# Performance work log

Hardware: AMD Instinct MI355X
Metric: run time of the kernel (lower is better)

The kernel has to match this reference:

```python
import jax, jax.numpy as jnp
import numpy as np

E = 1024
H = 16
D = E // H  # head dim 64
B = 2
S = 2048


def setup_inputs() -> dict:
    key = jax.random.key(0)
    k1, k2, k3, k4, k5 = jax.random.split(key, 5)
    scale = 1.0 / np.sqrt(E)
    return {
        "x": jax.random.normal(k1, (B, S, E), dtype=jnp.float32),
        "W_in": jax.random.normal(k2, (E, 3 * E), dtype=jnp.float32) * scale,
        "b_in": jnp.zeros((3 * E,), dtype=jnp.float32),
        "W_out": jax.random.normal(k3, (E, E), dtype=jnp.float32) * scale,
        "b_out": jnp.zeros((E,), dtype=jnp.float32),
        "causal_mask": 1,
    }


def reference(x, W_in, b_in, W_out, b_out, causal_mask):
    b, s, e = x.shape
    qkv = x @ W_in + b_in                      # [B,S,3E]
    q, k, v = jnp.split(qkv, 3, axis=-1)
    # [B,S,E] -> [B,H,S,D]
    q = q.reshape(b, s, H, D).transpose(0, 2, 1, 3)
    k = k.reshape(b, s, H, D).transpose(0, 2, 1, 3)
    v = v.reshape(b, s, H, D).transpose(0, 2, 1, 3)
    scores = jnp.einsum("bhqd,bhkd->bhqk", q, k)
    if causal_mask:
        # mask applied before scaling in the original; -inf is scale-invariant
        mask = jnp.triu(jnp.ones((s, s), dtype=bool), k=1)
        scores = jnp.where(mask, -jnp.inf, scores)
    scores = scores / np.sqrt(D)
    weight = jax.nn.softmax(scores, axis=-1)
    out = jnp.einsum("bhqk,bhkd->bhqd", weight, v)   # [B,H,S,D]
    out = out.transpose(0, 2, 1, 3).reshape(b, s, e)
    return out @ W_out + b_out
```

## Files before the change

### kernel.cpp

```cpp
#include <hip/hip_runtime.h>
#include <hip/hip_bf16.h>
#include <cmath>

typedef __bf16 bf16;
typedef __attribute__((ext_vector_type(8))) __bf16 bf16x8;
typedef __attribute__((ext_vector_type(4))) __bf16 bf16x4;
typedef __attribute__((ext_vector_type(4))) float f32x4;
typedef __attribute__((ext_vector_type(16))) float f32x16;
typedef unsigned int u32;

constexpr int S  = 2048;
constexpr int E  = 1024;
constexpr int H  = 16;
constexpr int D  = 64;
constexpr int B  = 2;
constexpr int M  = B * S;
constexpr int N3 = 3 * E;
constexpr int NROWS = B * H * S;

static __device__ __forceinline__ void gload16(const void* g, void* l) {
  __builtin_amdgcn_global_load_lds((const __attribute__((address_space(1))) void*)g,
                                   (__attribute__((address_space(3))) void*)l, 16, 0, 0);
}

static __device__ __forceinline__ u32 pack2(float a, float b) {
  union { bf16 h[2]; u32 u; } r;
  r.h[0] = (bf16)a; r.h[1] = (bf16)b;
  return r.u;
}
typedef union { u32 w[4]; bf16x8 v; } FU;

__global__ void k_cvt(const float* __restrict__ in, bf16* __restrict__ out) {
  const int i = (blockIdx.x * blockDim.x + threadIdx.x) * 4;
  const float4 v = *(const float4*)(in + i);
  bf16x4 o = { (bf16)v.x, (bf16)v.y, (bf16)v.z, (bf16)v.w };
  *(bf16x4*)(out + i) = o;
}

__global__ void k_transpose_cvt(const float* __restrict__ in, bf16* __restrict__ out,
                                int R, int C) {
  __shared__ float t[32][33];
  const int c0 = blockIdx.x * 32, r0 = blockIdx.y * 32;
  const int tx = threadIdx.x, ty = threadIdx.y;
  #pragma unroll
  for (int j = 0; j < 32; j += 8)
    t[ty + j][tx] = in[(size_t)(r0 + ty + j) * C + c0 + tx];
  __syncthreads();
  #pragma unroll
  for (int j = 0; j < 32; j += 8)
    out[(size_t)(c0 + ty + j) * R + r0 + tx] = (bf16)t[tx][ty + j];
}

template<int EPI>
__global__ __launch_bounds__(256) void k_gemm(
    const bf16* __restrict__ A, const bf16* __restrict__ Bt,
    const float* __restrict__ bias, float* __restrict__ outF,
    bf16* __restrict__ oQ, bf16* __restrict__ oK, bf16* __restrict__ oV,
    int Kdim, int Nn)
{
  __shared__ __align__(16) char smem[65536];
  const int tid = threadIdx.x;
  const int lane = tid & 63, w = tid >> 6;
  const int lane15 = lane & 15, quad = lane >> 4;
  const int wm = w >> 1, wn = w & 1;

  const int nbx = Nn >> 7;
  const int nwg = gridDim.x;
  const int bid = blockIdx.x;
  const int swz = (bid & 7) * (nwg >> 3) + (bid >> 3);
  const int bn0 = (swz % nbx) * 128;
  const int bm0 = (swz / nbx) * 128;

  const int so0 = w * 1024 + lane * 16;
  int srow[4], slk[4];
  #pragma unroll
  for (int p = 0; p < 4; ++p) {
    const int o = p * 4096 + so0;
    const int row = o >> 7, cbyte = o & 127;
    srow[p] = row;
    slk[p] = (cbyte ^ ((row & 7) << 4)) >> 1;
  }

  f32x4 acc[4][4] = {};
  const int nkt = Kdim >> 6;

  #pragma unroll
  for (int p = 0; p < 4; ++p) {
    gload16(A  + (size_t)(bm0 + srow[p]) * Kdim + slk[p], smem +         p * 4096 + w * 1024);
    gload16(Bt + (size_t)(bn0 + srow[p]) * Kdim + slk[p], smem + 32768 + p * 4096 + w * 1024);
  }

  #pragma unroll 1
  for (int kt = 0; kt < nkt; ++kt) {
    const int cur = kt & 1;
    __builtin_amdgcn_s_barrier();
    if (kt + 1 < nkt) {
      const int k0 = (kt + 1) << 6;
      const int nb = (cur ^ 1) * 16384;
      #pragma unroll
      for (int p = 0; p < 4; ++p) {
        gload16(A  + (size_t)(bm0 + srow[p]) * Kdim + k0 + slk[p],
                smem + nb +         p * 4096 + w * 1024);
        gload16(Bt + (size_t)(bn0 + srow[p]) * Kdim + k0 + slk[p],
                smem + nb + 32768 + p * 4096 + w * 1024);
      }
      asm volatile("s_waitcnt vmcnt(8)" ::: "memory");
    } else {
      asm volatile("s_waitcnt vmcnt(0)" ::: "memory");
    }
    __builtin_amdgcn_s_barrier();

    const char* cA = smem + cur * 16384;
    const char* cB = smem + 32768 + cur * 16384;
    #pragma unroll
    for (int kk = 0; kk < 2; ++kk) {
      bf16x8 af[4], bfr[4];
      #pragma unroll
      for (int f = 0; f < 4; ++f) {
        const int ra = wm * 64 + f * 16 + lane15;
        af[f] = *(const bf16x8*)(cA + ra * 128 +
                 ((kk * 64 + (quad << 4)) ^ ((ra & 7) << 4)));
        const int rb = wn * 64 + f * 16 + lane15;
        bfr[f] = *(const bf16x8*)(cB + rb * 128 +
                 ((kk * 64 + (quad << 4)) ^ ((rb & 7) << 4)));
      }
      #pragma unroll
      for (int i = 0; i < 4; ++i)
        #pragma unroll
        for (int j = 0; j < 4; ++j)
          acc[i][j] = __builtin_amdgcn_mfma_f32_16x16x32_bf16(af[i], bfr[j], acc[i][j], 0, 0, 0);
    }
  }

  if constexpr (EPI == 1) {
    #pragma unroll
    for (int i = 0; i < 4; ++i)
      #pragma unroll
      for (int j = 0; j < 4; ++j) {
        const int n = bn0 + wn * 64 + j * 16 + lane15;
        const float bv = bias[n];
        #pragma unroll
        for (int r = 0; r < 4; ++r) {
          const int m = bm0 + wm * 64 + i * 16 + quad * 4 + r;
          outF[(size_t)m * E + n] = acc[i][j][r] + bv;
        }
      }
  } else {
    const int which = bn0 >> 10;
    const int b  = bm0 >> 11;
    const int s0 = bm0 & (S - 1);
    const int cn0 = bn0 & (E - 1);
    if (which < 2) {
      __builtin_amdgcn_s_barrier();
      char* lC = smem;
      #pragma unroll
      for (int j = 0; j < 4; ++j) {
        const int n_loc = wn * 64 + j * 16 + lane15;
        const float bv = bias[bn0 + n_loc];
        #pragma unroll
        for (int i = 0; i < 4; ++i)
          #pragma unroll
          for (int r = 0; r < 4; ++r) {
            const int m_loc = wm * 64 + i * 16 + quad * 4 + r;
            *(bf16*)(lC + m_loc * 256 + ((n_loc * 2) ^ ((m_loc & 7) << 4))) =
                (bf16)(acc[i][j][r] + bv);
          }
      }
      __builtin_amdgcn_s_barrier();
      const int h0 = cn0 >> 6;
      #pragma unroll
      for (int it = 0; it < 8; ++it) {
        const int cch = w * 64 + it * 8 + (lane >> 3);
        const int m_loc = cch >> 1, hh = cch & 1, piece = lane & 7;
        const bf16x8 vv = *(const bf16x8*)(lC + m_loc * 256 +
                          ((hh * 128 + piece * 16) ^ ((m_loc & 7) << 4)));
        if (which == 0) {
          *(bf16x8*)(oQ + ((size_t)(b * H + h0 + hh) * S + s0 + m_loc) * D + piece * 8) = vv;
        } else {
          const size_t hb = (size_t)(b * H + h0 + hh) * S * D;
          const int tile = (s0 + m_loc) >> 6;
          const int row = m_loc & 63;
          *(bf16x8*)(oK + hb + (size_t)tile * 4096 + (piece >> 1) * 1024 +
                     (row >> 5) * 512 + (32 * (piece & 1) + (row & 31)) * 8) = vv;
        }
      }
    } else {
      #pragma unroll
      for (int j = 0; j < 4; ++j) {
        const int n_loc = wn * 64 + j * 16 + lane15;
        const int cn = cn0 + n_loc;
        const int hv = cn >> 6, dd = cn & 63;
        const float bv = bias[bn0 + n_loc];
        const size_t hb = (size_t)(b * H + hv) * S * D;
        #pragma unroll
        for (int i = 0; i < 4; ++i) {
          const int scol_g = s0 + wm * 64 + i * 16 + quad * 4;
          const int vtile = scol_g >> 6;
          const int cg = (scol_g & 63) >> 3;
          bf16x4 pk = { (bf16)(acc[i][j][0] + bv), (bf16)(acc[i][j][1] + bv),
                        (bf16)(acc[i][j][2] + bv), (bf16)(acc[i][j][3] + bv) };
          *(bf16x4*)(oV + hb + (size_t)vtile * 4096 + (cg >> 1) * 1024 +
                     (dd >> 5) * 512 + (32 * (cg & 1) + (dd & 31)) * 8 +
                     (quad & 1) * 4) = pk;
        }
      }
    }
  }
}

__global__ __launch_bounds__(256, 2) void k_attn(
    const bf16* __restrict__ Qb, const bf16* __restrict__ Kf, const bf16* __restrict__ Vf,
    bf16* __restrict__ pO0, bf16* __restrict__ pO1,
    float* __restrict__ pM, float* __restrict__ pL, const int* __restrict__ cmask)
{
  __shared__ float corr_lds[4][32];
  __shared__ float lrow_lds[4][32];

  const int tid = threadIdx.x, lane = tid & 63, w = tid >> 6;
  const int h = lane >> 5, q31 = lane & 31;
  const int bh = blockIdx.x;
  const int jb = blockIdx.y;
  const int causal = cmask[0];
  const float S2 = 0.18033688011112042f;

  const bf16* Qh = Qb + (size_t)bh * S * D;
  const bf16* Kh = Kf + (size_t)bh * S * D;
  const bf16* Vh = Vf + (size_t)bh * S * D;

  #pragma unroll 1
  for (int pidx = 0; pidx < 2; ++pidx) {
    const int c  = pidx ? (15 - jb) : jb;
    const int t0 = causal ? (pidx ? (c + 1) : 0) : (pidx ? 16 : 0);
    const int t1 = causal ? (pidx ? (2 * c + 2) : (c + 1)) : (pidx ? 32 : 16);
    const int q0w = c * 128 + 32 * w;
    const int qg  = q0w + q31;
    const int t1w = causal ? min(t1, (q0w + 31) / 64 + 1) : t1;

    bf16x8 qf[4];
    #pragma unroll
    for (int ds = 0; ds < 4; ++ds)
      qf[ds] = *(const bf16x8*)(Qh + (size_t)qg * D + 16 * ds + 8 * h);

    f32x16 o0 = {}, o1 = {};
    float mrun = -INFINITY, lr = 0.f;

    #pragma unroll 1
    for (int t = t0; t < t1w; ++t) {
      const bf16* ktb = Kh + (size_t)t * 4096;
      const bf16* vtb = Vh + (size_t)t * 4096;

      bf16x8 kf0[4], kf1[4];
      #pragma unroll
      for (int ds = 0; ds < 4; ++ds) {
        kf0[ds] = *(const bf16x8*)(ktb + ds * 1024 +       lane * 8);
        kf1[ds] = *(const bf16x8*)(ktb + ds * 1024 + 512 + lane * 8);
      }

      f32x16 s0v = {}, s1v = {};
      __builtin_amdgcn_s_setprio(1);
      #pragma unroll
      for (int ds = 0; ds < 4; ++ds) {
        s0v = __builtin_amdgcn_mfma_f32_32x32x16_bf16(kf0[ds], qf[ds], s0v, 0, 0, 0);
        s1v = __builtin_amdgcn_mfma_f32_32x32x16_bf16(kf1[ds], qf[ds], s1v, 0, 0, 0);
      }
      __builtin_amdgcn_s_setprio(0);

      if (causal && (64 * t + 63 > q0w)) {
        #pragma unroll
        for (int r = 0; r < 16; ++r) {
          const int kg = 64 * t + (r & 3) + 8 * (r >> 2) + 4 * h;
          if (kg > qg)      s0v[r] = -INFINITY;
          if (kg + 32 > qg) s1v[r] = -INFINITY;
        }
      }

      float a8[8];
      #pragma unroll
      for (int i = 0; i < 8; ++i)
        a8[i] = fmaxf(fmaxf(s0v[i], s0v[i + 8]), fmaxf(s1v[i], s1v[i + 8]));
      float tmax = fmaxf(fmaxf(fmaxf(a8[0], a8[1]), fmaxf(a8[2], a8[3])),
                         fmaxf(fmaxf(a8[4], a8[5]), fmaxf(a8[6], a8[7])));
      tmax = fmaxf(tmax, __shfl_xor(tmax, 32, 64));

      const bool nogrow = __all(tmax <= mrun);
      const float mnew = nogrow ? mrun : fmaxf(mrun, tmax);
      float corrf = 1.f;
      if (!nogrow) {
        corrf = __builtin_amdgcn_exp2f((mrun - mnew) * S2);
        corr_lds[w][q31] = corrf;
      }
      const float msc = mnew * S2;

      #pragma unroll
      for (int r = 0; r < 16; ++r) {
        s0v[r] = __builtin_amdgcn_exp2f(__builtin_fmaf(s0v[r], S2, -msc));
        s1v[r] = __builtin_amdgcn_exp2f(__builtin_fmaf(s1v[r], S2, -msc));
      }

      float b8[8];
      #pragma unroll
      for (int i = 0; i < 8; ++i)
        b8[i] = (s0v[i] + s0v[i + 8]) + (s1v[i] + s1v[i + 8]);
      float psum = ((b8[0] + b8[1]) + (b8[2] + b8[3])) + ((b8[4] + b8[5]) + (b8[6] + b8[7]));
      psum += __shfl_xor(psum, 32, 64);
      lr = lr * corrf + psum;
      mrun = mnew;

      u32 pk[8][2];
      #pragma unroll
      for (int jj = 0; jj < 4; ++jj) {
        pk[jj][0]     = pack2(s0v[4 * jj],     s0v[4 * jj + 1]);
        pk[jj][1]     = pack2(s0v[4 * jj + 2], s0v[4 * jj + 3]);
        pk[jj + 4][0] = pack2(s1v[4 * jj],     s1v[4 * jj + 1]);
        pk[jj + 4][1] = pack2(s1v[4 * jj + 2], s1v[4 * jj + 3]);
      }

      if (!nogrow) {
        #pragma unroll
        for (int j = 0; j < 4; ++j) {
          const f32x4 cv = *(const f32x4*)&corr_lds[w][8 * j + 4 * h];
          #pragma unroll
          for (int sr = 0; sr < 4; ++sr) {
            o0[4 * j + sr] *= cv[sr];
            o1[4 * j + sr] *= cv[sr];
          }
        }
      }

      __builtin_amdgcn_s_setprio(1);
      #pragma unroll
      for (int ks = 0; ks < 4; ++ks) {
        u32 a0 = pk[2 * ks][0], b0 = pk[2 * ks + 1][0];
        u32 a1 = pk[2 * ks][1], b1 = pk[2 * ks + 1][1];
        asm volatile("v_permlane32_swap_b32 %0, %1" : "+v"(a0), "+v"(b0));
        asm volatile("v_permlane32_swap_b32 %0, %1" : "+v"(a1), "+v"(b1));
        FU f; f.w[0] = a0; f.w[1] = a1; f.w[2] = b0; f.w[3] = b1;
        const bf16x8 vf0 = *(const bf16x8*)(vtb + ks * 1024 +       lane * 8);
        const bf16x8 vf1 = *(const bf16x8*)(vtb + ks * 1024 + 512 + lane * 8);
        o0 = __builtin_amdgcn_mfma_f32_32x32x16_bf16(f.v, vf0, o0, 0, 0, 0);
        o1 = __builtin_amdgcn_mfma_f32_32x32x16_bf16(f.v, vf1, o1, 0, 0, 0);
      }
      __builtin_amdgcn_s_setprio(0);
    }

    if (h == 0) {
      pM[(size_t)pidx * NROWS + bh * S + qg] = mrun;
      pL[(size_t)pidx * NROWS + bh * S + qg] = lr;
    }
    lrow_lds[w][q31] = lr;
    bf16* po = pidx ? pO1 : pO0;
    #pragma unroll
    for (int j = 0; j < 4; ++j) {
      const f32x4 lv = *(const f32x4*)&lrow_lds[w][8 * j + 4 * h];
      #pragma unroll
      for (int sr = 0; sr < 4; ++sr) {
        const int r = 4 * j + sr;
        const float inv = lv[sr] > 0.f ? 1.0f / lv[sr] : 0.f;
        const int qrow = q0w + (r & 3) + 8 * (r >> 2) + 4 * h;
        bf16* dst = po + ((size_t)(bh * S + qrow)) * D;
        dst[q31]      = (bf16)(o0[r] * inv);
        dst[32 + q31] = (bf16)(o1[r] * inv);
      }
    }
  }
}

__global__ __launch_bounds__(256) void k_combine(
    const bf16* __restrict__ pO0, const bf16* __restrict__ pO1,
    const float* __restrict__ pM, const float* __restrict__ pL,
    bf16* __restrict__ AO)
{
  const float S2 = 0.18033688011112042f;
  const int idx = blockIdx.x * 256 + threadIdx.x;
  const int row = idx >> 3, d0 = (idx & 7) * 8;
  const float mA = pM[row], mB = pM[NROWS + row];
  const float lA = pL[row], lB = pL[NROWS + row];
  const float m = fmaxf(mA, mB);
  const float wA = lA > 0.f ? lA * __builtin_amdgcn_exp2f((mA - m) * S2) : 0.f;
  const float wB = lB > 0.f ? lB * __builtin_amdgcn_exp2f((mB - m) * S2) : 0.f;
  const float inv = 1.0f / (wA + wB);
  const bf16x8 a = *(const bf16x8*)(pO0 + (size_t)row * D + d0);
  const bf16x8 b = *(const bf16x8*)(pO1 + (size_t)row * D + d0);
  bf16x8 o;
  #pragma unroll
  for (int i = 0; i < 8; ++i)
    o[i] = (bf16)((wA * (float)a[i] + wB * (float)b[i]) * inv);
  const int bb = row >> 15, hh = (row >> 11) & 15, s = row & 2047;
  *(bf16x8*)(AO + ((size_t)(bb * S + s)) * E + hh * D + d0) = o;
}

extern "C" void kernel_launch(void* const* d_in, const int* in_sizes, int n_in,
                              void* d_out, int out_size, void* d_ws, size_t ws_size,
                              hipStream_t stream) {
  (void)in_sizes; (void)n_in; (void)out_size; (void)ws_size;
  const float* x     = (const float*)d_in[0];
  const float* W_in  = (const float*)d_in[1];
  const float* b_in  = (const float*)d_in[2];
  const float* W_out = (const float*)d_in[3];
  const float* b_out = (const float*)d_in[4];
  const int*   cmask = (const int*)d_in[5];

  char* ws = (char*)d_ws;
  bf16* xb    = (bf16*)ws; ws += (size_t)M * E * 2;
  bf16* wtin  = (bf16*)ws; ws += (size_t)N3 * E * 2;
  bf16* wtout = (bf16*)ws; ws += (size_t)E * E * 2;
  bf16* qB    = (bf16*)ws; ws += (size_t)B * H * S * D * 2;
  bf16* kF    = (bf16*)ws; ws += (size_t)B * H * S * D * 2;
  bf16* vF    = (bf16*)ws; ws += (size_t)B * H * S * D * 2;
  bf16* ao    = (bf16*)ws; ws += (size_t)M * E * 2;
  bf16* pO1   = (bf16*)ws; ws += (size_t)NROWS * D * 2;
  float* pMb  = (float*)ws; ws += (size_t)2 * NROWS * 4;
  float* pLb  = (float*)ws; ws += (size_t)2 * NROWS * 4;
  bf16* pO0   = xb;

  k_cvt<<<M * E / 1024, 256, 0, stream>>>(x, xb);
  k_transpose_cvt<<<dim3(N3 / 32, E / 32), dim3(32, 8), 0, stream>>>(W_in, wtin, E, N3);
  k_transpose_cvt<<<dim3(E / 32, E / 32), dim3(32, 8), 0, stream>>>(W_out, wtout, E, E);
  k_gemm<0><<<dim3((M / 128) * (N3 / 128)), 256, 0, stream>>>(
      xb, wtin, b_in, nullptr, qB, kF, vF, E, N3);
  k_attn<<<dim3(32, 16), 256, 0, stream>>>(qB, kF, vF, pO0, pO1, pMb, pLb, cmask);
  k_combine<<<NROWS * 8 / 256, 256, 0, stream>>>(pO0, pO1, pMb, pLb, ao);
  k_gemm<1><<<dim3((M / 128) * (E / 128)), 256, 0, stream>>>(
      ao, wtout, b_out, (float*)d_out, nullptr, nullptr, nullptr, E, E);
}
```

Baseline: 117.0 us.

## Split attention pair loop into separate blocks and raise occupancy

Each attention block previously ran two KV-range partitions in sequence, one per query chunk pair. Now every partition gets its own block (grid doubled to 32x32), with heavy chunks scheduled first, and launch bounds raised to 4 waves per SIMD. The goal is more parallelism and better latency hiding across the CUs. The cost is possible register pressure or spills under the tighter bound, and losing the load balancing that the pairing gave each block.

```diff
diff --git a/kernel.cpp b/kernel.cpp
--- a/kernel.cpp
+++ b/kernel.cpp
@@ -208,7 +208,7 @@
   }
 }
 
-__global__ __launch_bounds__(256, 2) void k_attn(
+__global__ __launch_bounds__(256, 4) void k_attn(
     const bf16* __restrict__ Qb, const bf16* __restrict__ Kf, const bf16* __restrict__ Vf,
     bf16* __restrict__ pO0, bf16* __restrict__ pO1,
     float* __restrict__ pM, float* __restrict__ pL, const int* __restrict__ cmask)
@@ -219,7 +219,9 @@
   const int tid = threadIdx.x, lane = tid & 63, w = tid >> 6;
   const int h = lane >> 5, q31 = lane & 31;
   const int bh = blockIdx.x;
-  const int jb = blockIdx.y;
+  const int yy = blockIdx.y;
+  const int pidx = yy & 1;
+  const int c = 15 - (yy >> 1);
   const int causal = cmask[0];
   const float S2 = 0.18033688011112042f;
 
@@ -227,140 +229,136 @@
   const bf16* Kh = Kf + (size_t)bh * S * D;
   const bf16* Vh = Vf + (size_t)bh * S * D;
 
+  const int t0 = causal ? (pidx ? (c + 1) : 0) : (pidx ? 16 : 0);
+  const int t1 = causal ? (pidx ? (2 * c + 2) : (c + 1)) : (pidx ? 32 : 16);
+  const int q0w = c * 128 + 32 * w;
+  const int qg  = q0w + q31;
+  const int t1w = causal ? min(t1, ((q0w + 31) >> 6) + 1) : t1;
+
+  bf16x8 qf[4];
+  #pragma unroll
+  for (int ds = 0; ds < 4; ++ds)
+    qf[ds] = *(const bf16x8*)(Qh + (size_t)qg * D + 16 * ds + 8 * h);
+
+  f32x16 o0 = {}, o1 = {};
+  float mrun = -INFINITY, lr = 0.f;
+
   #pragma unroll 1
-  for (int pidx = 0; pidx < 2; ++pidx) {
-    const int c  = pidx ? (15 - jb) : jb;
-    const int t0 = causal ? (pidx ? (c + 1) : 0) : (pidx ? 16 : 0);
-    const int t1 = causal ? (pidx ? (2 * c + 2) : (c + 1)) : (pidx ? 32 : 16);
-    const int q0w = c * 128 + 32 * w;
-    const int qg  = q0w + q31;
-    const int t1w = causal ? min(t1, (q0w + 31) / 64 + 1) : t1;
-
-    bf16x8 qf[4];
-    #pragma unroll
-    for (int ds = 0; ds < 4; ++ds)
-      qf[ds] = *(const bf16x8*)(Qh + (size_t)qg * D + 16 * ds + 8 * h);
-
-    f32x16 o0 = {}, o1 = {};
-    float mrun = -INFINITY, lr = 0.f;
-
-    #pragma unroll 1
-    for (int t = t0; t < t1w; ++t) {
-      const bf16* ktb = Kh + (size_t)t * 4096;
-      const bf16* vtb = Vh + (size_t)t * 4096;
-
-      bf16x8 kf0[4], kf1[4];
-      #pragma unroll
-      for (int ds = 0; ds < 4; ++ds) {
-        kf0[ds] = *(const bf16x8*)(ktb + ds * 1024 +       lane * 8);
-        kf1[ds] = *(const bf16x8*)(ktb + ds * 1024 + 512 + lane * 8);
-      }
-
-      f32x16 s0v = {}, s1v = {};
-      __builtin_amdgcn_s_setprio(1);
-      #pragma unroll
-      for (int ds = 0; ds < 4; ++ds) {
-        s0v = __builtin_amdgcn_mfma_f32_32x32x16_bf16(kf0[ds], qf[ds], s0v, 0, 0, 0);
-        s1v = __builtin_amdgcn_mfma_f32_32x32x16_bf16(kf1[ds], qf[ds], s1v, 0, 0, 0);
-      }
-      __builtin_amdgcn_s_setprio(0);
-
-      if (causal && (64 * t + 63 > q0w)) {
+  for (int t = t0; t < t1w; ++t) {
+    const bf16* ktb = Kh + (size_t)t * 4096;
+    const bf16* vtb = Vh + (size_t)t * 4096;
+
+    bf16x8 kf0[4], kf1[4];
+    #pragma unroll
+    for (int ds = 0; ds < 4; ++ds) {
+      kf0[ds] = *(const bf16x8*)(ktb + ds * 1024 +       lane * 8);
+      kf1[ds] = *(const bf16x8*)(ktb + ds * 1024 + 512 + lane * 8);
+    }
+
+    f32x16 s0v = {}, s1v = {};
+    __builtin_amdgcn_s_setprio(1);
+    #pragma unroll
+    for (int ds = 0; ds < 4; ++ds) {
+      s0v = __builtin_amdgcn_mfma_f32_32x32x16_bf16(kf0[ds], qf[ds], s0v, 0, 0, 0);
+      s1v = __builtin_amdgcn_mfma_f32_32x32x16_bf16(kf1[ds], qf[ds], s1v, 0, 0, 0);
+    }
+    __builtin_amdgcn_s_setprio(0);
+
+    if (causal && (64 * t + 63 > q0w)) {
+      #pragma unroll
+      for (int rr = 0; rr < 16; ++rr) {
+        const int kg = 64 * t + (rr & 3) + 8 * (rr >> 2) + 4 * h;
+        if (kg > qg)      s0v[rr] = -INFINITY;
+        if (kg + 32 > qg) s1v[rr] = -INFINITY;
+      }
+    }
+
+    float a8[8];
+    #pragma unroll
+    for (int i = 0; i < 8; ++i)
+      a8[i] = fmaxf(fmaxf(s0v[i], s0v[i + 8]), fmaxf(s1v[i], s1v[i + 8]));
+    float tmax = fmaxf(fmaxf(fmaxf(a8[0], a8[1]), fmaxf(a8[2], a8[3])),
+                       fmaxf(fmaxf(a8[4], a8[5]), fmaxf(a8[6], a8[7])));
+    tmax = fmaxf(tmax, __shfl_xor(tmax, 32, 64));
+
+    const bool nogrow = __all(tmax <= mrun);
+    const float mnew = nogrow ? mrun : fmaxf(mrun, tmax);
+    float corrf = 1.f;
+    if (!nogrow) {
+      corrf = __builtin_amdgcn_exp2f((mrun - mnew) * S2);
+      corr_lds[w][q31] = corrf;
+    }
+    const float msc = mnew * S2;
+
+    #pragma unroll
+    for (int rr = 0; rr < 16; ++rr) {
+      s0v[rr] = __builtin_amdgcn_exp2f(__builtin_fmaf(s0v[rr], S2, -msc));
+      s1v[rr] = __builtin_amdgcn_exp2f(__builtin_fmaf(s1v[rr], S2, -msc));
+    }
+
+    float b8[8];
+    #pragma unroll
+    for (int i = 0; i < 8; ++i)
+      b8[i] = (s0v[i] + s0v[i + 8]) + (s1v[i] + s1v[i + 8]);
+    float psum = ((b8[0] + b8[1]) + (b8[2] + b8[3])) + ((b8[4] + b8[5]) + (b8[6] + b8[7]));
+    psum += __shfl_xor(psum, 32, 64);
+    lr = lr * corrf + psum;
+    mrun = mnew;
+
+    u32 pk[8][2];
+    #pragma unroll
+    for (int jj = 0; jj < 4; ++jj) {
+      pk[jj][0]     = pack2(s0v[4 * jj],     s0v[4 * jj + 1]);
+      pk[jj][1]     = pack2(s0v[4 * jj + 2], s0v[4 * jj + 3]);
+      pk[jj + 4][0] = pack2(s1v[4 * jj],     s1v[4 * jj + 1]);
+      pk[jj + 4][1] = pack2(s1v[4 * jj + 2], s1v[4 * jj + 3]);
+    }
+
+    if (!nogrow) {
+      #pragma unroll
+      for (int j = 0; j < 4; ++j) {
+        const f32x4 cv = *(const f32x4*)&corr_lds[w][8 * j + 4 * h];
         #pragma unroll
-        for (int r = 0; r < 16; ++r) {
-          const int kg = 64 * t + (r & 3) + 8 * (r >> 2) + 4 * h;
-          if (kg > qg)      s0v[r] = -INFINITY;
-          if (kg + 32 > qg) s1v[r] = -INFINITY;
+        for (int sr = 0; sr < 4; ++sr) {
+          o0[4 * j + sr] *= cv[sr];
+          o1[4 * j + sr] *= cv[sr];
         }
       }
-
-      float a8[8];
-      #pragma unroll
-      for (int i = 0; i < 8; ++i)
-        a8[i] = fmaxf(fmaxf(s0v[i], s0v[i + 8]), fmaxf(s1v[i], s1v[i + 8]));
-      float tmax = fmaxf(fmaxf(fmaxf(a8[0], a8[1]), fmaxf(a8[2], a8[3])),
-                         fmaxf(fmaxf(a8[4], a8[5]), fmaxf(a8[6], a8[7])));
-      tmax = fmaxf(tmax, __shfl_xor(tmax, 32, 64));
-
-      const bool nogrow = __all(tmax <= mrun);
-      const float mnew = nogrow ? mrun : fmaxf(mrun, tmax);
-      float corrf = 1.f;
-      if (!nogrow) {
-        corrf = __builtin_amdgcn_exp2f((mrun - mnew) * S2);
-        corr_lds[w][q31] = corrf;
-      }
-      const float msc = mnew * S2;
-
-      #pragma unroll
-      for (int r = 0; r < 16; ++r) {
-        s0v[r] = __builtin_amdgcn_exp2f(__builtin_fmaf(s0v[r], S2, -msc));
-        s1v[r] = __builtin_amdgcn_exp2f(__builtin_fmaf(s1v[r], S2, -msc));
-      }
-
-      float b8[8];
-      #pragma unroll
-      for (int i = 0; i < 8; ++i)
-        b8[i] = (s0v[i] + s0v[i + 8]) + (s1v[i] + s1v[i + 8]);
-      float psum = ((b8[0] + b8[1]) + (b8[2] + b8[3])) + ((b8[4] + b8[5]) + (b8[6] + b8[7]));
-      psum += __shfl_xor(psum, 32, 64);
-      lr = lr * corrf + psum;
-      mrun = mnew;
-
-      u32 pk[8][2];
-      #pragma unroll
-      for (int jj = 0; jj < 4; ++jj) {
-        pk[jj][0]     = pack2(s0v[4 * jj],     s0v[4 * jj + 1]);
-        pk[jj][1]     = pack2(s0v[4 * jj + 2], s0v[4 * jj + 3]);
-        pk[jj + 4][0] = pack2(s1v[4 * jj],     s1v[4 * jj + 1]);
-        pk[jj + 4][1] = pack2(s1v[4 * jj + 2], s1v[4 * jj + 3]);
-      }
-
-      if (!nogrow) {
-        #pragma unroll
-        for (int j = 0; j < 4; ++j) {
-          const f32x4 cv = *(const f32x4*)&corr_lds[w][8 * j + 4 * h];
-          #pragma unroll
-          for (int sr = 0; sr < 4; ++sr) {
-            o0[4 * j + sr] *= cv[sr];
-            o1[4 * j + sr] *= cv[sr];
-          }
-        }
-      }
-
-      __builtin_amdgcn_s_setprio(1);
-      #pragma unroll
-      for (int ks = 0; ks < 4; ++ks) {
-        u32 a0 = pk[2 * ks][0], b0 = pk[2 * ks + 1][0];
-        u32 a1 = pk[2 * ks][1], b1 = pk[2 * ks + 1][1];
-        asm volatile("v_permlane32_swap_b32 %0, %1" : "+v"(a0), "+v"(b0));
-        asm volatile("v_permlane32_swap_b32 %0, %1" : "+v"(a1), "+v"(b1));
-        FU f; f.w[0] = a0; f.w[1] = a1; f.w[2] = b0; f.w[3] = b1;
-        const bf16x8 vf0 = *(const bf16x8*)(vtb + ks * 1024 +       lane * 8);
-        const bf16x8 vf1 = *(const bf16x8*)(vtb + ks * 1024 + 512 + lane * 8);
-        o0 = __builtin_amdgcn_mfma_f32_32x32x16_bf16(f.v, vf0, o0, 0, 0, 0);
-        o1 = __builtin_amdgcn_mfma_f32_32x32x16_bf16(f.v, vf1, o1, 0, 0, 0);
-      }
-      __builtin_amdgcn_s_setprio(0);
-    }
-
-    if (h == 0) {
-      pM[(size_t)pidx * NROWS + bh * S + qg] = mrun;
-      pL[(size_t)pidx * NROWS + bh * S + qg] = lr;
-    }
-    lrow_lds[w][q31] = lr;
-    bf16* po = pidx ? pO1 : pO0;
-    #pragma unroll
-    for (int j = 0; j < 4; ++j) {
-      const f32x4 lv = *(const f32x4*)&lrow_lds[w][8 * j + 4 * h];
-      #pragma unroll
-      for (int sr = 0; sr < 4; ++sr) {
-        const int r = 4 * j + sr;
-        const float inv = lv[sr] > 0.f ? 1.0f / lv[sr] : 0.f;
-        const int qrow = q0w + (r & 3) + 8 * (r >> 2) + 4 * h;
-        bf16* dst = po + ((size_t)(bh * S + qrow)) * D;
-        dst[q31]      = (bf16)(o0[r] * inv);
-        dst[32 + q31] = (bf16)(o1[r] * inv);
-      }
+    }
+
+    __builtin_amdgcn_s_setprio(1);
+    #pragma unroll
+    for (int ks = 0; ks < 4; ++ks) {
+      u32 a0 = pk[2 * ks][0], b0 = pk[2 * ks + 1][0];
+      u32 a1 = pk[2 * ks][1], b1 = pk[2 * ks + 1][1];
+      asm volatile("v_permlane32_swap_b32 %0, %1" : "+v"(a0), "+v"(b0));
+      asm volatile("v_permlane32_swap_b32 %0, %1" : "+v"(a1), "+v"(b1));
+      FU f; f.w[0] = a0; f.w[1] = a1; f.w[2] = b0; f.w[3] = b1;
+      const bf16x8 vf0 = *(const bf16x8*)(vtb + ks * 1024 +       lane * 8);
+      const bf16x8 vf1 = *(const bf16x8*)(vtb + ks * 1024 + 512 + lane * 8);
+      o0 = __builtin_amdgcn_mfma_f32_32x32x16_bf16(f.v, vf0, o0, 0, 0, 0);
+      o1 = __builtin_amdgcn_mfma_f32_32x32x16_bf16(f.v, vf1, o1, 0, 0, 0);
+    }
+    __builtin_amdgcn_s_setprio(0);
+  }
+
+  if (h == 0) {
+    pM[(size_t)pidx * NROWS + bh * S + qg] = mrun;
+    pL[(size_t)pidx * NROWS + bh * S + qg] = lr;
+  }
+  lrow_lds[w][q31] = lr;
+  bf16* po = pidx ? pO1 : pO0;
+  #pragma unroll
+  for (int j = 0; j < 4; ++j) {
+    const f32x4 lv = *(const f32x4*)&lrow_lds[w][8 * j + 4 * h];
+    #pragma unroll
+    for (int sr = 0; sr < 4; ++sr) {
+      const int rr = 4 * j + sr;
+      const float inv = lv[sr] > 0.f ? 1.0f / lv[sr] : 0.f;
+      const int qrow = q0w + (rr & 3) + 8 * (rr >> 2) + 4 * h;
+      bf16* dst = po + ((size_t)(bh * S + qrow)) * D;
+      dst[q31]      = (bf16)(o0[rr] * inv);
+      dst[32 + q31] = (bf16)(o1[rr] * inv);
     }
   }
 }
@@ -418,7 +416,7 @@
   k_transpose_cvt<<<dim3(E / 32, E / 32), dim3(32, 8), 0, stream>>>(W_out, wtout, E, E);
   k_gemm<0><<<dim3((M / 128) * (N3 / 128)), 256, 0, stream>>>(
       xb, wtin, b_in, nullptr, qB, kF, vF, E, N3);
-  k_attn<<<dim3(32, 16), 256, 0, stream>>>(qB, kF, vF, pO0, pO1, pMb, pLb, cmask);
+  k_attn<<<dim3(32, 32), 256, 0, stream>>>(qB, kF, vF, pO0, pO1, pMb, pLb, cmask);
   k_combine<<<NROWS * 8 / 256, 256, 0, stream>>>(pO0, pO1, pMb, pLb, ao);
   k_gemm<1><<<dim3((M / 128) * (E / 128)), 256, 0, stream>>>(
       ao, wtout, b_out, (float*)d_out, nullptr, nullptr, nullptr, E, E);
```

Measured after the change: 114.4 us. -2.2%, faster.
